# Optimization experiments

Hardware: AMD Instinct MI355X
Metric: run time of the kernel (lower is better)

## Reference

```python
import jax, jax.numpy as jnp
import numpy as np

N_ENT = 50000
N_REL = 16
D_E = 64
D_R = 64
D_OUT = 32
N_EDGE = 1000000


def setup_inputs() -> dict:
    key = jax.random.key(0)
    ks = jax.random.split(key, 8)
    # 0.1 scale keeps tanh / softmax in a realistic (non-saturated) range,
    # mimicking trained embedding magnitudes.
    entity_table = jax.random.normal(ks[0], (N_ENT, D_E), dtype=jnp.float32) * 0.1
    relation_table = jax.random.normal(ks[1], (N_REL, D_R), dtype=jnp.float32) * 0.1
    W_R = jax.random.normal(ks[2], (N_REL, D_E, D_R), dtype=jnp.float32) * (1.0 / np.sqrt(D_E))
    W1 = jax.random.normal(ks[3], (D_E, D_OUT), dtype=jnp.float32) * (1.0 / np.sqrt(D_E))
    b1 = jnp.zeros((D_OUT,), dtype=jnp.float32)
    W2 = jax.random.normal(ks[4], (D_E, D_OUT), dtype=jnp.float32) * (1.0 / np.sqrt(D_E))
    b2 = jnp.zeros((D_OUT,), dtype=jnp.float32)
    src = jax.random.randint(ks[5], (N_EDGE,), 0, N_ENT, dtype=jnp.int32)
    dst = jax.random.randint(ks[6], (N_EDGE,), 0, N_ENT, dtype=jnp.int32)
    etype = jax.random.randint(ks[7], (N_EDGE,), 0, N_REL, dtype=jnp.int32)
    return {"entity_table": entity_table, "relation_table": relation_table,
            "W_R": W_R, "W1": W1, "b1": b1, "W2": W2, "b2": b2,
            "src": src, "dst": dst, "etype": etype}


def reference(entity_table, relation_table, W_R, W1, b1, W2, b2, src, dst, etype):
    """KGAT calc_att (per-relation edge attention + edge softmax) followed by
    one bi-interaction Aggregator layer (dropout = identity, eval mode)."""
    n_nodes = entity_table.shape[0]
    # Per-relation projection of all node embeddings (grouped GEMM form of the
    # per-relation loop in compute_attention): [R, N, d_r]
    proj = jnp.einsum('nd,rde->rne', entity_table, W_R)
    r_mul_h = proj[etype, src]            # [E, d_r]  h W_r per edge
    r_mul_t = proj[etype, dst]            # [E, d_r]  t W_r per edge
    r_e = relation_table[etype]           # [E, d_r]
    # att = (h W_r) . tanh(t W_r + r)
    att = jnp.sum(r_mul_h * jnp.tanh(r_mul_t + r_e), axis=-1)  # [E]
    # edge softmax grouped by destination node
    att_max = jax.ops.segment_max(att, dst, num_segments=n_nodes)     # [N]
    ex = jnp.exp(att - att_max[dst])
    denom = jax.ops.segment_sum(ex, dst, num_segments=n_nodes)        # [N]
    a = ex / denom[dst]                                               # [E]
    # u_mul_e + sum: N_h[v] = sum_{(u->v)} a_e * node[u]
    msg = a[:, None] * entity_table[src]                              # [E, d]
    N_h = jax.ops.segment_sum(msg, dst, num_segments=n_nodes)         # [N, d]
    node = entity_table
    # bi-interaction aggregator (LeakyReLU slope 0.01, torch default)
    out1 = jax.nn.leaky_relu((node + N_h) @ W1 + b1)
    out2 = jax.nn.leaky_relu((node * N_h) @ W2 + b2)
    return out1 + out2
```

## Files before the change

kernel.cpp:

```cpp
#include <hip/hip_runtime.h>
#include <math.h>

#define NREL 16
#define DE 64
#define DOUT 32
#define NPART 8
#define TQ 392

typedef __attribute__((ext_vector_type(8))) short bf16x8;
typedef __attribute__((ext_vector_type(16))) float f32x16;
typedef __attribute__((ext_vector_type(2))) float f32x2;

__device__ __forceinline__ short f2bf(float f) {
    unsigned u = __builtin_bit_cast(unsigned, f);
    unsigned r = (u + 0x7FFFu + ((u >> 16) & 1u)) >> 16;
    return (short)r;
}
__device__ __forceinline__ float bf2f(short s) {
    unsigned u = ((unsigned)(unsigned short)s) << 16;
    return __builtin_bit_cast(float, u);
}
__device__ __forceinline__ unsigned char f2fp8(float f) {
    int p = __builtin_amdgcn_cvt_pk_fp8_f32(f, f, 0, false);
    return (unsigned char)(p & 0xff);
}
__device__ __forceinline__ float tanh_fast(float x) {
    float e = __expf(2.0f * x);
    return fmaf(-2.0f, __builtin_amdgcn_rcpf(e + 1.0f), 1.0f);
}

__global__ __launch_bounds__(256) void prep_kernel(const float* __restrict__ ent,
                                                   short* __restrict__ entbf, int eTot,
                                                   const float* __restrict__ WR,
                                                   short* __restrict__ Wbf,
                                                   short* __restrict__ WTbf,
                                                   const int* __restrict__ dst,
                                                   int* __restrict__ counts,
                                                   int E, int psz,
                                                   int eB, int wB) {
    int b = blockIdx.x;
    if (b < eB) {
        int i = b * 256 + threadIdx.x;
        if (i < eTot) entbf[i] = f2bf(ent[i]);
    } else if (b < eB + wB) {
        int i = (b - eB) * 256 + threadIdx.x;
        int r = i >> 12, k = (i >> 6) & 63, j = i & 63;
        short w = f2bf(WR[i]);
        Wbf[i] = w;
        WTbf[(r << 12) + (j << 6) + k] = w;
    } else {
        int hb = b - eB - wB;
        int part = hb & (NPART - 1);
        int i = (hb >> 3) * 256 + threadIdx.x;
        if (i < E) {
            int d = dst[i];
            if (d >= part * psz && d < (part + 1) * psz)
                atomicAdd(&counts[d], 1);
        }
    }
}

__global__ __launch_bounds__(256) void blocksum_kernel(const int* __restrict__ counts,
                                                       int* __restrict__ blockSums, int n) {
    __shared__ int wsum[4];
    int i = blockIdx.x * 256 + threadIdx.x;
    int v = (i < n) ? counts[i] : 0;
#pragma unroll
    for (int off = 1; off < 64; off <<= 1) v += __shfl_xor(v, off);
    if ((threadIdx.x & 63) == 0) wsum[threadIdx.x >> 6] = v;
    __syncthreads();
    if (threadIdx.x == 0)
        blockSums[blockIdx.x] = wsum[0] + wsum[1] + wsum[2] + wsum[3];
}

__global__ __launch_bounds__(1024) void blockscan_kernel(int* __restrict__ blockSums, int nb) {
    __shared__ int lds[1024];
    int t = threadIdx.x;
    int v = (t < nb) ? blockSums[t] : 0;
    lds[t] = v;
    __syncthreads();
    for (int off = 1; off < 1024; off <<= 1) {
        int u = (t >= off) ? lds[t - off] : 0;
        __syncthreads();
        lds[t] += u;
        __syncthreads();
    }
    if (t < nb) blockSums[t] = (t == 0) ? 0 : lds[t - 1];
}

__global__ __launch_bounds__(256) void scanout_kernel(const int* __restrict__ counts,
                                                      const int* __restrict__ blockSums,
                                                      int* __restrict__ offsets,
                                                      int* __restrict__ cursor, int n) {
    __shared__ int wsum[4];
    int t = threadIdx.x;
    int i = blockIdx.x * 256 + t;
    int lane = t & 63;
    int w = t >> 6;
    int v = (i < n) ? counts[i] : 0;
    int incl = v;
#pragma unroll
    for (int off = 1; off < 64; off <<= 1) {
        int u = __shfl_up(incl, off);
        if (lane >= off) incl += u;
    }
    if (lane == 63) wsum[w] = incl;
    __syncthreads();
    int woff = 0;
#pragma unroll
    for (int j = 0; j < 4; ++j) if (j < w) woff += wsum[j];
    int excl = incl - v + woff + blockSums[blockIdx.x];
    if (i < n) { offsets[i] = excl; cursor[i] = excl; }
    if (i == n - 1) offsets[n] = excl + v;
}

__global__ __launch_bounds__(256) void projscat_kernel(const short* __restrict__ entbf,
                                                       const float* __restrict__ rel,
                                                       const short* __restrict__ Wbf,
                                                       const short* __restrict__ WTbf,
                                                       unsigned char* __restrict__ Qf8,
                                                       int N, int nProj,
                                                       const int* __restrict__ dst,
                                                       const int* __restrict__ src,
                                                       const int* __restrict__ etype,
                                                       int* __restrict__ cursor,
                                                       int* __restrict__ pks,
                                                       int E, int psz) {
    __shared__ short Tl[4 * 2048];
    if ((int)blockIdx.x >= nProj) {
        int sb = blockIdx.x - nProj;
        int part = sb & (NPART - 1);
        int i = (sb >> 3) * 256 + threadIdx.x;
        if (i < E) {
            int d = dst[i];
            if (d >= part * psz && d < (part + 1) * psz) {
                int pos = atomicAdd(&cursor[d], 1);
                pks[pos] = (src[i] << 4) | etype[i];
            }
        }
        return;
    }
    int lane = threadIdx.x & 63;
    int wid = threadIdx.x >> 6;
    int lin = blockIdx.x;
    int r = lin / TQ;
    int tq = lin - r * TQ;
    int m0 = (tq * 4 + wid) * 32;
    if (m0 >= N) return;
    int hi = lane >> 5;
    int lo = lane & 31;

    int arow = m0 + lo;
    if (arow >= N) arow = N - 1;
    const short* ap = entbf + ((size_t)arow << 6) + hi * 8;
    bf16x8 A[4];
#pragma unroll
    for (int kk = 0; kk < 4; ++kk) A[kk] = *(const bf16x8*)(ap + kk * 16);

    short* tb = Tl + wid * 2048;
    const short* wtb = WTbf + ((size_t)r << 12);
    const short* wb  = Wbf  + ((size_t)r << 12);

    f32x16 acc0 = {}, acc1 = {};
#pragma unroll
    for (int kk = 0; kk < 4; ++kk) {
        bf16x8 b0 = *(const bf16x8*)(wtb + lo * DE + kk * 16 + hi * 8);
        bf16x8 b1 = *(const bf16x8*)(wtb + (lo + 32) * DE + kk * 16 + hi * 8);
        acc0 = __builtin_amdgcn_mfma_f32_32x32x16_bf16(A[kk], b0, acc0, 0, 0, 0);
        acc1 = __builtin_amdgcn_mfma_f32_32x32x16_bf16(A[kk], b1, acc1, 0, 0, 0);
    }
    float rv0 = rel[r * DE + lo];
    float rv1 = rel[r * DE + 32 + lo];
#pragma unroll
    for (int i = 0; i < 16; ++i) {
        int row = (i & 3) + 8 * (i >> 2) + 4 * hi;
        int sw = (row & 7) << 3;
        tb[(row * DE + lo) ^ sw] = f2bf(tanh_fast(acc0[i] + rv0));
        tb[(row * DE + 32 + lo) ^ sw] = f2bf(tanh_fast(acc1[i] + rv1));
    }
    bf16x8 A2[4];
#pragma unroll
    for (int kk = 0; kk < 4; ++kk)
        A2[kk] = *(const bf16x8*)(tb + ((lo * DE + kk * 16 + hi * 8) ^ ((lo & 7) << 3)));

    f32x16 q0 = {}, q1 = {};
#pragma unroll
    for (int kk = 0; kk < 4; ++kk) {
        bf16x8 b0 = *(const bf16x8*)(wb + lo * DE + kk * 16 + hi * 8);
        bf16x8 b1 = *(const bf16x8*)(wb + (lo + 32) * DE + kk * 16 + hi * 8);
        q0 = __builtin_amdgcn_mfma_f32_32x32x16_bf16(A2[kk], b0, q0, 0, 0, 0);
        q1 = __builtin_amdgcn_mfma_f32_32x32x16_bf16(A2[kk], b1, q1, 0, 0, 0);
    }
    unsigned char* tb8 = (unsigned char*)tb;
#pragma unroll
    for (int i = 0; i < 16; ++i) {
        int row = (i & 3) + 8 * (i >> 2) + 4 * hi;
        tb8[row * DE + lo] = f2fp8(q0[i]);
        tb8[row * DE + 32 + lo] = f2fp8(q1[i]);
    }
#pragma unroll
    for (int p = 0; p < 4; ++p) {
        int row = p * 8 + (lane >> 3);
        int node = m0 + row;
        unsigned long long vq = *(const unsigned long long*)(tb8 + row * DE + (lane & 7) * 8);
        if (node < N)
            *(unsigned long long*)(Qf8 + (((size_t)r * N + node) << 6) + (lane & 7) * 8) = vq;
    }
}

__global__ __launch_bounds__(256) void agg_kernel(const float* __restrict__ ent,
                                                  const short* __restrict__ entbf,
                                                  const unsigned char* __restrict__ Qf8,
                                                  const int* __restrict__ offsets,
                                                  const int* __restrict__ pks,
                                                  const float* __restrict__ W1,
                                                  const float* __restrict__ b1,
                                                  const float* __restrict__ W2,
                                                  const float* __restrict__ b2,
                                                  float* __restrict__ out, int n) {
    __shared__ float xl[4][128];
    int lane = threadIdx.x & 63;
    int wid = threadIdx.x >> 6;
    int v = (blockIdx.x << 2) + wid;
    if (v >= n) return;
    int o0 = offsets[v], o1 = offsets[v + 1];
    int g = lane >> 3, gl = lane & 7;
    const unsigned char* qbase = Qf8 + ((size_t)v << 6) + gl * 8;

    float m = -INFINITY, l = 0.f;
    float acc[8];
#pragma unroll
    for (int j = 0; j < 8; ++j) acc[j] = 0.f;

    int k = o0 + g;
    bool val = k < o1;
    bf16x8 xv = {};
    uint2 qv = {};
    if (val) {
        int pk = pks[k];
        xv = *(const bf16x8*)(entbf + ((size_t)(pk >> 4) << 6) + gl * 8);
        qv = *(const uint2*)(qbase + (((size_t)(pk & 15) * (size_t)n) << 6));
    }
    int iters = (o1 - o0 + 7) >> 3;
    for (int it = 0; it < iters; ++it) {
        int kn = k + 8;
        bool valn = kn < o1;
        bf16x8 xn = {};
        uint2 qn = {};
        if (valn) {
            int pk = pks[kn];
            xn = *(const bf16x8*)(entbf + ((size_t)(pk >> 4) << 6) + gl * 8);
            qn = *(const uint2*)(qbase + (((size_t)(pk & 15) * (size_t)n) << 6));
        }
        f32x2 qa = __builtin_amdgcn_cvt_pk_f32_fp8(qv.x, false);
        f32x2 qb = __builtin_amdgcn_cvt_pk_f32_fp8(qv.x, true);
        f32x2 qc = __builtin_amdgcn_cvt_pk_f32_fp8(qv.y, false);
        f32x2 qd = __builtin_amdgcn_cvt_pk_f32_fp8(qv.y, true);
        float qf[8] = {qa[0], qa[1], qb[0], qb[1], qc[0], qc[1], qd[0], qd[1]};
        float xf[8];
        float d = 0.f;
#pragma unroll
        for (int j = 0; j < 8; ++j) {
            xf[j] = bf2f(xv[j]);
            d = fmaf(xf[j], qf[j], d);
        }
        d += __shfl_xor(d, 1);
        d += __shfl_xor(d, 2);
        d += __shfl_xor(d, 4);
        float p = val ? d : -INFINITY;
        float nm = fmaxf(m, p);
        float sc, pe;
        if (nm == -INFINITY) { sc = 0.f; pe = 0.f; }
        else { sc = __expf(m - nm); pe = __expf(p - nm); }
        l = l * sc + pe;
#pragma unroll
        for (int j = 0; j < 8; ++j) acc[j] = fmaf(acc[j], sc, pe * xf[j]);
        m = nm;
        k = kn; val = valn; xv = xn; qv = qn;
    }
#pragma unroll
    for (int off = 8; off < 64; off <<= 1) {
        float mo = __shfl_xor(m, off);
        float lo2 = __shfl_xor(l, off);
        float nm = fmaxf(m, mo);
        float s1 = (nm == -INFINITY) ? 0.f : __expf(m - nm);
        float s2 = (nm == -INFINITY) ? 0.f : __expf(mo - nm);
        l = l * s1 + lo2 * s2;
#pragma unroll
        for (int j = 0; j < 8; ++j) {
            float ao = __shfl_xor(acc[j], off);
            acc[j] = acc[j] * s1 + ao * s2;
        }
        m = nm;
    }
    float* xw = &xl[wid][0];
    float invl = (l > 0.f) ? (1.0f / l) : 0.f;
    if (g == 0) {
#pragma unroll
        for (int j = 0; j < 8; ++j) xw[gl * 8 + j] = acc[j] * invl;
    }
    float node = ent[((size_t)v << 6) + lane];
    float Nh = xw[lane];
    float x1 = node + Nh;
    float x2 = node * Nh;
    xw[lane] = x1;
    xw[64 + lane] = x2;
    int j = lane & 31;
    const float* __restrict__ Wsel = (lane < 32) ? W1 : W2;
    float bias = (lane < 32) ? b1[j] : b2[j];
    const float* xb = xw + ((lane < 32) ? 0 : 64);
    float o = 0.f;
#pragma unroll 8
    for (int kk = 0; kk < DE; ++kk)
        o = fmaf(xb[kk], Wsel[kk * DOUT + j], o);
    o += bias;
    float lr = (o > 0.f) ? o : 0.01f * o;
    float other = __shfl_xor(lr, 32);
    if (lane < 32) out[(size_t)v * DOUT + lane] = lr + other;
}

extern "C" void kernel_launch(void* const* d_in, const int* in_sizes, int n_in,
                              void* d_out, int out_size, void* d_ws, size_t ws_size,
                              hipStream_t stream) {
    const float* ent = (const float*)d_in[0];
    const float* rel = (const float*)d_in[1];
    const float* WR  = (const float*)d_in[2];
    const float* W1  = (const float*)d_in[3];
    const float* b1  = (const float*)d_in[4];
    const float* W2  = (const float*)d_in[5];
    const float* b2  = (const float*)d_in[6];
    const int* src   = (const int*)d_in[7];
    const int* dst   = (const int*)d_in[8];
    const int* ety   = (const int*)d_in[9];
    float* out       = (float*)d_out;

    const int E = in_sizes[7];
    const int N = in_sizes[0] / DE;
    const int NB = (N + 255) / 256;
    const int psz = (N + NPART - 1) / NPART;
    const int chunks = (E + 255) / 256;

    size_t qBytes  = (size_t)N * NREL * DE;
    size_t eElems  = (size_t)N * DE;
    size_t wElems  = (size_t)NREL * DE * DE;

    char* ws = (char*)d_ws;
    unsigned char* Qf8 = (unsigned char*)ws;
    short* entbf = (short*)(ws + qBytes);
    short* Wbf   = entbf + eElems;
    short* WTbf  = Wbf + wElems;
    int* counts  = (int*)(WTbf + wElems);
    int* offsets = counts + N;
    int* cursor  = offsets + N + 1;
    int* pks     = cursor + N;
    int* bsums   = pks + E;
    size_t need  = (size_t)((char*)(bsums + NB) - ws);
    if (ws_size < need) return;

    const int eB = (int)((eElems + 255) / 256);
    const int wB = (int)(wElems / 256);
    const int nProj = TQ * NREL;

    hipMemsetAsync(counts, 0, (size_t)N * 4, stream);
    prep_kernel<<<eB + wB + chunks * NPART, 256, 0, stream>>>(
        ent, entbf, (int)eElems, WR, Wbf, WTbf, dst, counts, E, psz, eB, wB);
    blocksum_kernel<<<NB, 256, 0, stream>>>(counts, bsums, N);
    blockscan_kernel<<<1, 1024, 0, stream>>>(bsums, NB);
    scanout_kernel<<<NB, 256, 0, stream>>>(counts, bsums, offsets, cursor, N);
    projscat_kernel<<<nProj + chunks * NPART, 256, 0, stream>>>(
        entbf, rel, Wbf, WTbf, Qf8, N, nProj, dst, src, ety, cursor, pks, E, psz);
    agg_kernel<<<(N + 3) / 4, 256, 0, stream>>>(ent, entbf, Qf8, offsets, pks,
                                                W1, b1, W2, b2, out, N);
}
```

Measured before the change: 222.1 us.

## Split projection/scatter kernels, double partitions, prefetch edge keys deeper

```diff
diff --git a/kernel.cpp b/kernel.cpp
--- a/kernel.cpp
+++ b/kernel.cpp
@@ -4,7 +4,7 @@
 #define NREL 16
 #define DE 64
 #define DOUT 32
-#define NPART 8
+#define NPART 16
 #define TQ 392
 
 typedef __attribute__((ext_vector_type(8))) short bf16x8;
@@ -51,7 +51,7 @@
     } else {
         int hb = b - eB - wB;
         int part = hb & (NPART - 1);
-        int i = (hb >> 3) * 256 + threadIdx.x;
+        int i = (hb / NPART) * 256 + threadIdx.x;
         if (i < E) {
             int d = dst[i];
             if (d >= part * psz && d < (part + 1) * psz)
@@ -114,32 +114,30 @@
     if (i == n - 1) offsets[n] = excl + v;
 }
 
-__global__ __launch_bounds__(256) void projscat_kernel(const short* __restrict__ entbf,
-                                                       const float* __restrict__ rel,
-                                                       const short* __restrict__ Wbf,
-                                                       const short* __restrict__ WTbf,
-                                                       unsigned char* __restrict__ Qf8,
-                                                       int N, int nProj,
-                                                       const int* __restrict__ dst,
-                                                       const int* __restrict__ src,
-                                                       const int* __restrict__ etype,
-                                                       int* __restrict__ cursor,
-                                                       int* __restrict__ pks,
-                                                       int E, int psz) {
+__global__ __launch_bounds__(256) void scatter_kernel(const int* __restrict__ dst,
+                                                      const int* __restrict__ src,
+                                                      const int* __restrict__ etype,
+                                                      int* __restrict__ cursor,
+                                                      int* __restrict__ pks,
+                                                      int E, int psz) {
+    int part = blockIdx.x & (NPART - 1);
+    int i = (blockIdx.x / NPART) * 256 + threadIdx.x;
+    if (i < E) {
+        int d = dst[i];
+        if (d >= part * psz && d < (part + 1) * psz) {
+            int pos = atomicAdd(&cursor[d], 1);
+            pks[pos] = (src[i] << 4) | etype[i];
+        }
+    }
+}
+
+__global__ __launch_bounds__(256) void projq_kernel(const short* __restrict__ entbf,
+                                                    const float* __restrict__ rel,
+                                                    const short* __restrict__ Wbf,
+                                                    const short* __restrict__ WTbf,
+                                                    unsigned char* __restrict__ Qf8,
+                                                    int N) {
     __shared__ short Tl[4 * 2048];
-    if ((int)blockIdx.x >= nProj) {
-        int sb = blockIdx.x - nProj;
-        int part = sb & (NPART - 1);
-        int i = (sb >> 3) * 256 + threadIdx.x;
-        if (i < E) {
-            int d = dst[i];
-            if (d >= part * psz && d < (part + 1) * psz) {
-                int pos = atomicAdd(&cursor[d], 1);
-                pks[pos] = (src[i] << 4) | etype[i];
-            }
-        }
-        return;
-    }
     int lane = threadIdx.x & 63;
     int wid = threadIdx.x >> 6;
     int lin = blockIdx.x;
@@ -204,7 +202,8 @@
         int node = m0 + row;
         unsigned long long vq = *(const unsigned long long*)(tb8 + row * DE + (lane & 7) * 8);
         if (node < N)
-            *(unsigned long long*)(Qf8 + (((size_t)r * N + node) << 6) + (lane & 7) * 8) = vq;
+            __builtin_nontemporal_store(vq,
+                (unsigned long long*)(Qf8 + (((size_t)r * N + node) << 6) + (lane & 7) * 8));
     }
 }
 
@@ -241,17 +240,22 @@
         xv = *(const bf16x8*)(entbf + ((size_t)(pk >> 4) << 6) + gl * 8);
         qv = *(const uint2*)(qbase + (((size_t)(pk & 15) * (size_t)n) << 6));
     }
+    int kn = k + 8;
+    bool valn = kn < o1;
+    int pkn = valn ? pks[kn] : 0;
+
     int iters = (o1 - o0 + 7) >> 3;
     for (int it = 0; it < iters; ++it) {
-        int kn = k + 8;
-        bool valn = kn < o1;
         bf16x8 xn = {};
         uint2 qn = {};
         if (valn) {
-            int pk = pks[kn];
-            xn = *(const bf16x8*)(entbf + ((size_t)(pk >> 4) << 6) + gl * 8);
-            qn = *(const uint2*)(qbase + (((size_t)(pk & 15) * (size_t)n) << 6));
-        }
+            xn = *(const bf16x8*)(entbf + ((size_t)(pkn >> 4) << 6) + gl * 8);
+            qn = *(const uint2*)(qbase + (((size_t)(pkn & 15) * (size_t)n) << 6));
+        }
+        int kn2 = kn + 8;
+        bool valn2 = kn2 < o1;
+        int pkn2 = valn2 ? pks[kn2] : 0;
+
         f32x2 qa = __builtin_amdgcn_cvt_pk_f32_fp8(qv.x, false);
         f32x2 qb = __builtin_amdgcn_cvt_pk_f32_fp8(qv.x, true);
         f32x2 qc = __builtin_amdgcn_cvt_pk_f32_fp8(qv.y, false);
@@ -276,7 +280,8 @@
 #pragma unroll
         for (int j = 0; j < 8; ++j) acc[j] = fmaf(acc[j], sc, pe * xf[j]);
         m = nm;
-        k = kn; val = valn; xv = xn; qv = qn;
+        val = valn; xv = xn; qv = qn;
+        kn = kn2; valn = valn2; pkn = pkn2;
     }
 #pragma unroll
     for (int off = 8; off < 64; off <<= 1) {
@@ -359,7 +364,6 @@
 
     const int eB = (int)((eElems + 255) / 256);
     const int wB = (int)(wElems / 256);
-    const int nProj = TQ * NREL;
 
     hipMemsetAsync(counts, 0, (size_t)N * 4, stream);
     prep_kernel<<<eB + wB + chunks * NPART, 256, 0, stream>>>(
@@ -367,8 +371,8 @@
     blocksum_kernel<<<NB, 256, 0, stream>>>(counts, bsums, N);
     blockscan_kernel<<<1, 1024, 0, stream>>>(bsums, NB);
     scanout_kernel<<<NB, 256, 0, stream>>>(counts, bsums, offsets, cursor, N);
-    projscat_kernel<<<nProj + chunks * NPART, 256, 0, stream>>>(
-        entbf, rel, Wbf, WTbf, Qf8, N, nProj, dst, src, ety, cursor, pks, E, psz);
+    scatter_kernel<<<chunks * NPART, 256, 0, stream>>>(dst, src, ety, cursor, pks, E, psz);
+    projq_kernel<<<TQ * NREL, 256, 0, stream>>>(entbf, rel, Wbf, WTbf, Qf8, N);
     agg_kernel<<<(N + 3) / 4, 256, 0, stream>>>(ent, entbf, Qf8, offsets, pks,
                                                 W1, b1, W2, b2, out, N);
 }
```

Result: slower. 237.4 us (+6.9%).
